# Performance work log

Hardware: AMD Instinct MI355X
Metric: run time of the kernel (lower is better)

## Reference

```python
import jax, jax.numpy as jnp
import numpy as np

B, L, E, H = 1, 2048, 512, 8
D = E // H


def setup_inputs() -> dict:
    key = jax.random.key(0)
    k0, k1, k2 = jax.random.split(key, 3)
    x = jax.random.normal(k0, (B, L, E), jnp.float32)
    W_qkv = jax.random.normal(k1, (E, 3 * E), jnp.float32) / np.sqrt(E).astype(np.float32)
    b_qkv = jnp.zeros((3 * E,), jnp.float32)
    W_out = jax.random.normal(k2, (E, E), jnp.float32) / np.sqrt(E).astype(np.float32)
    b_out = jnp.zeros((E,), jnp.float32)
    return {"x": x, "W_qkv": W_qkv, "b_qkv": b_qkv, "W_out": W_out, "b_out": b_out}


def reference(x, W_qkv, b_qkv, W_out, b_out):
    num_heads = H
    eps = 1e-6
    b, l, e = x.shape
    d = e // num_heads
    qkv = x @ W_qkv + b_qkv                      # [B, L, 3E]
    q, k, v = jnp.split(qkv, 3, axis=-1)
    q = q.reshape(b, l, num_heads, d).transpose(0, 2, 1, 3)  # [B,H,L,D]
    k = k.reshape(b, l, num_heads, d).transpose(0, 2, 1, 3)
    v = v.reshape(b, l, num_heads, d).transpose(0, 2, 1, 3)
    pos = jnp.arange(l, dtype=jnp.float32).reshape(1, 1, l, 1)
    cos_w = jnp.cos(jnp.pi / 2 * pos / l)
    sin_w = jnp.sin(jnp.pi / 2 * pos / l)
    q_prime = jax.nn.relu(q)
    k_prime = jax.nn.relu(k)

    def branch(w):
        qw = q_prime * w                          # [B,H,L,D]
        kw = k_prime * w
        kv = jnp.einsum('bhld,bhle->bhlde', kw, v)  # causal running KV state
        kv_cum = jnp.cumsum(kv, axis=2)
        ctx = jnp.einsum('bhld,bhlde->bhle', qw, kv_cum)
        nrm = jnp.einsum('bhld,bhld->bhl', qw, jnp.cumsum(kw, axis=2))
        return ctx, nrm

    ctx_cos, nrm_cos = branch(cos_w)
    ctx_sin, nrm_sin = branch(sin_w)
    out = (ctx_cos + ctx_sin) / ((nrm_cos + nrm_sin)[..., None] + eps)
    out = out.transpose(0, 2, 1, 3).reshape(b, l, e)
    return out @ W_out + b_out
```

## Files before the change

kernel.cpp:

```cpp
#include <hip/hip_runtime.h>

constexpr int L_SEQ = 2048;
constexpr int E_DIM = 512;
constexpr int H_NUM = 8;
constexpr int QKV_W = 3 * E_DIM;
constexpr int NC = 32;
constexpr float PI_HALF = 1.5707963267948966f;

typedef __attribute__((ext_vector_type(8))) short bf16x8;
typedef __attribute__((ext_vector_type(4))) float f32x4;
typedef __attribute__((ext_vector_type(4))) short short4v;

__device__ __forceinline__ short f2bf(float f) {
  union { float f; unsigned int u; } v; v.f = f;
  unsigned int r = v.u + 0x7fffu + ((v.u >> 16) & 1u);
  return (short)(r >> 16);
}
__device__ __forceinline__ float bf2f(short s) {
  union { unsigned int u; float f; } v;
  v.u = ((unsigned int)(unsigned short)s) << 16;
  return v.f;
}

__device__ __forceinline__ void glds16(const void* g, void* l) {
  __builtin_amdgcn_global_load_lds(
      (const __attribute__((address_space(1))) unsigned int*)g,
      (__attribute__((address_space(3))) unsigned int*)l, 16, 0, 0);
}

template <int WTM, int WTN, bool OB>
__global__ __launch_bounds__(256) void gemm_mfma_bf16(
    const short* __restrict__ A, const short* __restrict__ Bt,
    const float* __restrict__ bias, void* __restrict__ Cout,
    int M, int N, int K) {
  constexpr int BM = WTM * 32;
  constexpr int BN = WTN * 32;
  __shared__ short As[BM * 32];
  __shared__ short Bs[BN * 32];

  const int t = threadIdx.x;
  const int wave = t >> 6;
  const int lane = t & 63;
  const int quad = lane >> 4;
  const int lr = lane & 15;

  const int row0 = blockIdx.y * BM;
  const int col0 = blockIdx.x * BN;
  const int wrow = (wave >> 1) * (BM / 2);
  const int wcol = (wave & 1) * (BN / 2);

  f32x4 acc[WTM][WTN];
#pragma unroll
  for (int m = 0; m < WTM; ++m)
#pragma unroll
    for (int n = 0; n < WTN; ++n) acc[m][n] = (f32x4){0.f, 0.f, 0.f, 0.f};

  for (int k0 = 0; k0 < K; k0 += 32) {
#pragma unroll
    for (int p = wave; p < BM / 16; p += 4) {
      const int idx = p * 64 + lane;
      glds16(A + (size_t)(row0 + (idx >> 2)) * K + k0 + (idx & 3) * 8, As + p * 512);
    }
#pragma unroll
    for (int p = wave; p < BN / 16; p += 4) {
      const int idx = p * 64 + lane;
      glds16(Bt + (size_t)(col0 + (idx >> 2)) * K + k0 + (idx & 3) * 8, Bs + p * 512);
    }
    __syncthreads();

    bf16x8 af[WTM], bf_[WTN];
#pragma unroll
    for (int m = 0; m < WTM; ++m)
      af[m] = *(const bf16x8*)(As + (wrow + m * 16 + lr) * 32 + quad * 8);
#pragma unroll
    for (int n = 0; n < WTN; ++n)
      bf_[n] = *(const bf16x8*)(Bs + (wcol + n * 16 + lr) * 32 + quad * 8);
#pragma unroll
    for (int m = 0; m < WTM; ++m)
#pragma unroll
      for (int n = 0; n < WTN; ++n)
        acc[m][n] = __builtin_amdgcn_mfma_f32_16x16x32_bf16(af[m], bf_[n], acc[m][n], 0, 0, 0);
    __syncthreads();
  }

#pragma unroll
  for (int m = 0; m < WTM; ++m) {
#pragma unroll
    for (int n = 0; n < WTN; ++n) {
      const int col = col0 + wcol + n * 16 + lr;
      const int rowb = row0 + wrow + m * 16 + quad * 4;
      const float bb = bias[col];
#pragma unroll
      for (int r = 0; r < 4; ++r) {
        const float val = acc[m][n][r] + bb;
        if (OB)
          ((short*)Cout)[(size_t)(rowb + r) * N + col] = f2bf(val);
        else
          ((float*)Cout)[(size_t)(rowb + r) * N + col] = val;
      }
    }
  }
}

__global__ __launch_bounds__(256) void prep_kernel(
    const float* __restrict__ x, const float* __restrict__ W_qkv,
    const float* __restrict__ W_out, short* __restrict__ xb,
    short* __restrict__ Wqkv_t, short* __restrict__ Wout_t) {
  const int b = blockIdx.x;
  if (b < 1024) {
    const int i = b * 256 + threadIdx.x;
    const float4 v = ((const float4*)x)[i];
    short4v o;
    o.x = f2bf(v.x); o.y = f2bf(v.y); o.z = f2bf(v.z); o.w = f2bf(v.w);
    ((short4v*)xb)[i] = o;
    return;
  }
  __shared__ float tile[32][33];
  const float* W; short* Wt; int R, Cc, c0, r0;
  if (b < 1792) {
    const int bb = b - 1024;
    W = W_qkv; Wt = Wqkv_t; R = E_DIM; Cc = QKV_W;
    c0 = (bb % 48) * 32; r0 = (bb / 48) * 32;
  } else {
    const int bb = b - 1792;
    W = W_out; Wt = Wout_t; R = E_DIM; Cc = E_DIM;
    c0 = (bb % 16) * 32; r0 = (bb / 16) * 32;
  }
  const int tx = threadIdx.x & 31, ty = threadIdx.x >> 5;
  for (int i = ty; i < 32; i += 8) tile[i][tx] = W[(size_t)(r0 + i) * Cc + c0 + tx];
  __syncthreads();
  for (int i = ty; i < 32; i += 8)
    Wt[(size_t)(c0 + i) * R + r0 + tx] = f2bf(tile[tx][i]);
}

__global__ __launch_bounds__(256) void chunk_kv_mfma(
    const short* __restrict__ qkvb, short* __restrict__ Sb, float* __restrict__ ksum) {
  const int c = blockIdx.x, h = blockIdx.y;
  __shared__ short kT[128][72];
  __shared__ short vT[64][72];
  const int t = threadIdx.x;
  const int w = t >> 6, lane = t & 63, lr = lane & 15, quad = lane >> 4;

#pragma unroll
  for (int r = 0; r < 16; ++r) {
    const int i = w + 4 * r, d = lane;
    const short* row = qkvb + (size_t)(c * 64 + i) * QKV_W;
    const float kv_ = fmaxf(bf2f(row[E_DIM + h * 64 + d]), 0.f);
    const float v_ = bf2f(row[2 * E_DIM + h * 64 + d]);
    const float th = PI_HALF * (float)(c * 64 + i) / (float)L_SEQ;
    kT[d][i] = f2bf(kv_ * __cosf(th));
    kT[64 + d][i] = f2bf(kv_ * __sinf(th));
    vT[d][i] = f2bf(v_);
  }
  __syncthreads();

  f32x4 acc[8];
#pragma unroll
  for (int n = 0; n < 8; ++n) acc[n] = (f32x4){0.f, 0.f, 0.f, 0.f};
#pragma unroll
  for (int kk = 0; kk < 2; ++kk) {
    const bf16x8 av = *(const bf16x8*)&vT[16 * w + lr][kk * 32 + quad * 8];
#pragma unroll
    for (int n = 0; n < 8; ++n) {
      const bf16x8 bv = *(const bf16x8*)&kT[16 * n + lr][kk * 32 + quad * 8];
      acc[n] = __builtin_amdgcn_mfma_f32_16x16x32_bf16(av, bv, acc[n], 0, 0, 0);
    }
  }

  short* Sc = Sb + ((size_t)(h * NC + c)) * 8192;
#pragma unroll
  for (int n = 0; n < 8; ++n) {
    const int dd = 16 * n + lr;
#pragma unroll
    for (int r = 0; r < 4; ++r) {
      const int e = 16 * w + quad * 4 + r;
      Sc[(size_t)e * 128 + dd] = f2bf(acc[n][r]);
    }
  }

  if (t < 128) {
    float s = 0.f;
#pragma unroll
    for (int j = 0; j < 8; ++j) {
      const bf16x8 kv8 = *(const bf16x8*)&kT[t][j * 8];
#pragma unroll
      for (int q = 0; q < 8; ++q) s += bf2f(kv8[q]);
    }
    ksum[(size_t)(h * NC + c) * 128 + t] = s;
  }
}

__global__ __launch_bounds__(256) void scan_kernel(
    const short* __restrict__ Sb, short* __restrict__ Spb,
    const float* __restrict__ ksum, float* __restrict__ ksumP) {
  const int h = blockIdx.y;
  const int g = (blockIdx.x * 256 + threadIdx.x) * 8;
  float run[8];
#pragma unroll
  for (int q = 0; q < 8; ++q) run[q] = 0.f;
#pragma unroll
  for (int c = 0; c < NC; ++c) {
    const size_t off = ((size_t)(h * NC + c)) * 8192 + g;
    const bf16x8 v8 = *(const bf16x8*)(Sb + off);
    bf16x8 o;
#pragma unroll
    for (int q = 0; q < 8; ++q) o[q] = f2bf(run[q]);
    *(bf16x8*)(Spb + off) = o;
#pragma unroll
    for (int q = 0; q < 8; ++q) run[q] += bf2f(v8[q]);
  }
  if (blockIdx.x == 0 && threadIdx.x < 128) {
    const int d = threadIdx.x;
    float r2 = 0.f;
#pragma unroll
    for (int c = 0; c < NC; ++c) {
      const size_t off = (size_t)(h * NC + c) * 128 + d;
      ksumP[off] = r2;
      r2 += ksum[off];
    }
  }
}

__global__ __launch_bounds__(256) void chunk_out_mfma(
    const short* __restrict__ qkvb, const short* __restrict__ Spb,
    const float* __restrict__ ksumP, short* __restrict__ attn) {
  const int c = blockIdx.x, h = blockIdx.y;
  __shared__ short Qc[64][136];
  __shared__ short Kc[64][136];
  __shared__ short Am[64][72];
  __shared__ short vT[64][72];
  __shared__ float nrmP[64][4];
  __shared__ float nrmA[64];
  const int t = threadIdx.x;
  const int w = t >> 6, lane = t & 63, lr = lane & 15, quad = lane >> 4;

#pragma unroll
  for (int r = 0; r < 16; ++r) {
    const int i = w + 4 * r, d = lane;
    const short* row = qkvb + (size_t)(c * 64 + i) * QKV_W;
    const float q_ = fmaxf(bf2f(row[h * 64 + d]), 0.f);
    const float k_ = fmaxf(bf2f(row[E_DIM + h * 64 + d]), 0.f);
    const float v_ = bf2f(row[2 * E_DIM + h * 64 + d]);
    const float th = PI_HALF * (float)(c * 64 + i) / (float)L_SEQ;
    const float cw = __cosf(th), sw = __sinf(th);
    Qc[i][d] = f2bf(q_ * cw);
    Qc[i][64 + d] = f2bf(q_ * sw);
    Kc[i][d] = f2bf(k_ * cw);
    Kc[i][64 + d] = f2bf(k_ * sw);
    vT[d][i] = f2bf(v_);
  }
  __syncthreads();

  bf16x8 av[4];
#pragma unroll
  for (int kk = 0; kk < 4; ++kk)
    av[kk] = *(const bf16x8*)&Qc[16 * w + lr][kk * 32 + quad * 8];

  const short* Spc = Spb + ((size_t)(h * NC + c)) * 8192;
  f32x4 acc_c[4];
#pragma unroll
  for (int n = 0; n < 4; ++n) acc_c[n] = (f32x4){0.f, 0.f, 0.f, 0.f};
#pragma unroll
  for (int kk = 0; kk < 4; ++kk) {
#pragma unroll
    for (int n = 0; n < 4; ++n) {
      const bf16x8 bv = *(const bf16x8*)(Spc + (size_t)(16 * n + lr) * 128 + kk * 32 + quad * 8);
      acc_c[n] = __builtin_amdgcn_mfma_f32_16x16x32_bf16(av[kk], bv, acc_c[n], 0, 0, 0);
    }
  }

  f32x4 acc_a[4];
#pragma unroll
  for (int n = 0; n < 4; ++n) acc_a[n] = (f32x4){0.f, 0.f, 0.f, 0.f};
#pragma unroll
  for (int kk = 0; kk < 4; ++kk) {
#pragma unroll
    for (int n = 0; n < 4; ++n) {
      const bf16x8 bv = *(const bf16x8*)&Kc[16 * n + lr][kk * 32 + quad * 8];
      acc_a[n] = __builtin_amdgcn_mfma_f32_16x16x32_bf16(av[kk], bv, acc_a[n], 0, 0, 0);
    }
  }
#pragma unroll
  for (int n = 0; n < 4; ++n) {
#pragma unroll
    for (int r = 0; r < 4; ++r) {
      const int gi = 16 * w + quad * 4 + r;
      const int gj = 16 * n + lr;
      float val = (gj <= gi) ? acc_a[n][r] : 0.f;
      Am[gi][gj] = f2bf(val);
      float s = val;
      s += __shfl_xor(s, 1, 64);
      s += __shfl_xor(s, 2, 64);
      s += __shfl_xor(s, 4, 64);
      s += __shfl_xor(s, 8, 64);
      if (lr == 0) nrmP[gi][n] = s;
    }
  }
  __syncthreads();

#pragma unroll
  for (int kk = 0; kk < 2; ++kk) {
    const bf16x8 am = *(const bf16x8*)&Am[16 * w + lr][kk * 32 + quad * 8];
#pragma unroll
    for (int n = 0; n < 4; ++n) {
      const bf16x8 bv = *(const bf16x8*)&vT[16 * n + lr][kk * 32 + quad * 8];
      acc_c[n] = __builtin_amdgcn_mfma_f32_16x16x32_bf16(am, bv, acc_c[n], 0, 0, 0);
    }
  }

  {
    const int i = t >> 2, p = t & 3;
    const float* Kp = ksumP + (size_t)(h * NC + c) * 128;
    float dot = 0.f;
#pragma unroll
    for (int jj = 0; jj < 32; ++jj) {
      const int dd = p * 32 + jj;
      dot += bf2f(Qc[i][dd]) * Kp[dd];
    }
    nrmP[i][p] += dot;
  }
  __syncthreads();
  if (t < 64) nrmA[t] = nrmP[t][0] + nrmP[t][1] + nrmP[t][2] + nrmP[t][3];
  __syncthreads();

#pragma unroll
  for (int n = 0; n < 4; ++n) {
#pragma unroll
    for (int r = 0; r < 4; ++r) {
      const int gi = 16 * w + quad * 4 + r;
      const int e = 16 * n + lr;
      const float val = acc_c[n][r] / (nrmA[gi] + 1e-6f);
      attn[(size_t)(c * 64 + gi) * E_DIM + h * 64 + e] = f2bf(val);
    }
  }
}

extern "C" void kernel_launch(void* const* d_in, const int* in_sizes, int n_in,
                              void* d_out, int out_size, void* d_ws, size_t ws_size,
                              hipStream_t stream) {
  (void)in_sizes; (void)n_in; (void)out_size; (void)ws_size;
  const float* x     = (const float*)d_in[0];
  const float* W_qkv = (const float*)d_in[1];
  const float* b_qkv = (const float*)d_in[2];
  const float* W_out = (const float*)d_in[3];
  const float* b_out = (const float*)d_in[4];
  float* out = (float*)d_out;

  short* sws = (short*)d_ws;
  short* qkvb   = sws;
  short* Sb     = qkvb + 3145728;
  short* Spb    = Sb + 2097152;
  short* attn_b = Spb + 2097152;
  short* xb     = attn_b + 1048576;
  short* Wqkv_t = xb + 1048576;
  short* Wout_t = Wqkv_t + 786432;
  float* ksum   = (float*)(Wout_t + 262144);
  float* ksumP  = ksum + 32768;

  prep_kernel<<<2048, 256, 0, stream>>>(x, W_qkv, W_out, xb, Wqkv_t, Wout_t);

  gemm_mfma_bf16<2, 2, true><<<dim3(QKV_W / 64, L_SEQ / 64), 256, 0, stream>>>(
      xb, Wqkv_t, b_qkv, qkvb, L_SEQ, QKV_W, E_DIM);

  chunk_kv_mfma<<<dim3(NC, H_NUM), 256, 0, stream>>>(qkvb, Sb, ksum);

  scan_kernel<<<dim3(4, H_NUM), 256, 0, stream>>>(Sb, Spb, ksum, ksumP);

  chunk_out_mfma<<<dim3(NC, H_NUM), 256, 0, stream>>>(qkvb, Spb, ksumP, attn_b);

  gemm_mfma_bf16<1, 2, false><<<dim3(E_DIM / 64, L_SEQ / 32), 256, 0, stream>>>(
      attn_b, Wout_t, b_out, out, L_SEQ, E_DIM, E_DIM);
}
```

Baseline: 109.7 us.

## Split chunk KV and output kernels across a half dimension with vectorized loads

The chunk KV-state kernel and the chunk output kernel now launch twice as many blocks. The KV kernel splits the cos and sin halves across blocks, and the output kernel splits the value columns. Staging loads now use 8-wide bf16 vector reads with a single sincos call instead of scalar per-element loads. The aim is better occupancy of the many CUs on a small 256-block grid and cheaper global loads, at the cost of the output kernel recomputing the Q·K intra-chunk matrix and normalizer in both halves.

```diff
diff --git a/kernel.cpp b/kernel.cpp
--- a/kernel.cpp
+++ b/kernel.cpp
@@ -39,11 +39,7 @@
   __shared__ short Bs[BN * 32];
 
   const int t = threadIdx.x;
-  const int wave = t >> 6;
-  const int lane = t & 63;
-  const int quad = lane >> 4;
-  const int lr = lane & 15;
-
+  const int wave = t >> 6, lane = t & 63, quad = lane >> 4, lr = lane & 15;
   const int row0 = blockIdx.y * BM;
   const int col0 = blockIdx.x * BN;
   const int wrow = (wave >> 1) * (BM / 2);
@@ -116,69 +112,72 @@
     return;
   }
   __shared__ float tile[32][33];
-  const float* W; short* Wt; int R, Cc, c0, r0;
+  const float* W; short* Wt; int Cc, c0, r0;
   if (b < 1792) {
     const int bb = b - 1024;
-    W = W_qkv; Wt = Wqkv_t; R = E_DIM; Cc = QKV_W;
+    W = W_qkv; Wt = Wqkv_t; Cc = QKV_W;
     c0 = (bb % 48) * 32; r0 = (bb / 48) * 32;
   } else {
     const int bb = b - 1792;
-    W = W_out; Wt = Wout_t; R = E_DIM; Cc = E_DIM;
+    W = W_out; Wt = Wout_t; Cc = E_DIM;
     c0 = (bb % 16) * 32; r0 = (bb / 16) * 32;
   }
   const int tx = threadIdx.x & 31, ty = threadIdx.x >> 5;
   for (int i = ty; i < 32; i += 8) tile[i][tx] = W[(size_t)(r0 + i) * Cc + c0 + tx];
   __syncthreads();
   for (int i = ty; i < 32; i += 8)
-    Wt[(size_t)(c0 + i) * R + r0 + tx] = f2bf(tile[tx][i]);
-}
-
-__global__ __launch_bounds__(256) void chunk_kv_mfma(
+    Wt[(size_t)(c0 + i) * E_DIM + r0 + tx] = f2bf(tile[tx][i]);
+}
+
+__global__ __launch_bounds__(256) void chunk_kv_half(
     const short* __restrict__ qkvb, short* __restrict__ Sb, float* __restrict__ ksum) {
-  const int c = blockIdx.x, h = blockIdx.y;
-  __shared__ short kT[128][72];
+  const int c = blockIdx.x, h = blockIdx.y, half = blockIdx.z;
+  __shared__ short kT[64][72];
   __shared__ short vT[64][72];
   const int t = threadIdx.x;
-  const int w = t >> 6, lane = t & 63, lr = lane & 15, quad = lane >> 4;
-
-#pragma unroll
-  for (int r = 0; r < 16; ++r) {
-    const int i = w + 4 * r, d = lane;
-    const short* row = qkvb + (size_t)(c * 64 + i) * QKV_W;
-    const float kv_ = fmaxf(bf2f(row[E_DIM + h * 64 + d]), 0.f);
-    const float v_ = bf2f(row[2 * E_DIM + h * 64 + d]);
-    const float th = PI_HALF * (float)(c * 64 + i) / (float)L_SEQ;
-    kT[d][i] = f2bf(kv_ * __cosf(th));
-    kT[64 + d][i] = f2bf(kv_ * __sinf(th));
-    vT[d][i] = f2bf(v_);
-  }
-  __syncthreads();
-
-  f32x4 acc[8];
-#pragma unroll
-  for (int n = 0; n < 8; ++n) acc[n] = (f32x4){0.f, 0.f, 0.f, 0.f};
+  const int wave = t >> 6, lane = t & 63, quad = lane >> 4, lr = lane & 15;
+
+#pragma unroll
+  for (int r = 0; r < 2; ++r) {
+    const int idx = r * 256 + t;
+    const int i = idx >> 3, dg = idx & 7;
+    const short* row = qkvb + (size_t)(c * 64 + i) * QKV_W + h * 64 + dg * 8;
+    const bf16x8 kb = *(const bf16x8*)(row + E_DIM);
+    const bf16x8 vb = *(const bf16x8*)(row + 2 * E_DIM);
+    float sw, cw;
+    __sincosf(PI_HALF * (float)(c * 64 + i) / (float)L_SEQ, &sw, &cw);
+    const float wgt = half ? sw : cw;
+#pragma unroll
+    for (int q = 0; q < 8; ++q) {
+      kT[dg * 8 + q][i] = f2bf(fmaxf(bf2f(kb[q]), 0.f) * wgt);
+      vT[dg * 8 + q][i] = vb[q];
+    }
+  }
+  __syncthreads();
+
+  f32x4 sacc[4];
+#pragma unroll
+  for (int n = 0; n < 4; ++n) sacc[n] = (f32x4){0.f, 0.f, 0.f, 0.f};
 #pragma unroll
   for (int kk = 0; kk < 2; ++kk) {
-    const bf16x8 av = *(const bf16x8*)&vT[16 * w + lr][kk * 32 + quad * 8];
-#pragma unroll
-    for (int n = 0; n < 8; ++n) {
+    const bf16x8 av = *(const bf16x8*)&vT[16 * wave + lr][kk * 32 + quad * 8];
+#pragma unroll
+    for (int n = 0; n < 4; ++n) {
       const bf16x8 bv = *(const bf16x8*)&kT[16 * n + lr][kk * 32 + quad * 8];
-      acc[n] = __builtin_amdgcn_mfma_f32_16x16x32_bf16(av, bv, acc[n], 0, 0, 0);
-    }
-  }
-
+      sacc[n] = __builtin_amdgcn_mfma_f32_16x16x32_bf16(av, bv, sacc[n], 0, 0, 0);
+    }
+  }
   short* Sc = Sb + ((size_t)(h * NC + c)) * 8192;
 #pragma unroll
-  for (int n = 0; n < 8; ++n) {
-    const int dd = 16 * n + lr;
+  for (int n = 0; n < 4; ++n) {
+    const int dd = 64 * half + 16 * n + lr;
 #pragma unroll
     for (int r = 0; r < 4; ++r) {
-      const int e = 16 * w + quad * 4 + r;
-      Sc[(size_t)e * 128 + dd] = f2bf(acc[n][r]);
-    }
-  }
-
-  if (t < 128) {
+      const int e = 16 * wave + quad * 4 + r;
+      Sc[(size_t)e * 128 + dd] = f2bf(sacc[n][r]);
+    }
+  }
+  if (t < 64) {
     float s = 0.f;
 #pragma unroll
     for (int j = 0; j < 8; ++j) {
@@ -186,7 +185,7 @@
 #pragma unroll
       for (int q = 0; q < 8; ++q) s += bf2f(kv8[q]);
     }
-    ksum[(size_t)(h * NC + c) * 128 + t] = s;
+    ksum[(size_t)(h * NC + c) * 128 + 64 * half + t] = s;
   }
 }
 
@@ -221,53 +220,55 @@
   }
 }
 
-__global__ __launch_bounds__(256) void chunk_out_mfma(
+__global__ __launch_bounds__(256) void chunk_out_half(
     const short* __restrict__ qkvb, const short* __restrict__ Spb,
     const float* __restrict__ ksumP, short* __restrict__ attn) {
-  const int c = blockIdx.x, h = blockIdx.y;
+  const int c = blockIdx.x, h = blockIdx.y, eh = blockIdx.z;
   __shared__ short Qc[64][136];
   __shared__ short Kc[64][136];
   __shared__ short Am[64][72];
-  __shared__ short vT[64][72];
+  __shared__ short vT[32][72];
   __shared__ float nrmP[64][4];
   __shared__ float nrmA[64];
   const int t = threadIdx.x;
-  const int w = t >> 6, lane = t & 63, lr = lane & 15, quad = lane >> 4;
-
-#pragma unroll
-  for (int r = 0; r < 16; ++r) {
-    const int i = w + 4 * r, d = lane;
-    const short* row = qkvb + (size_t)(c * 64 + i) * QKV_W;
-    const float q_ = fmaxf(bf2f(row[h * 64 + d]), 0.f);
-    const float k_ = fmaxf(bf2f(row[E_DIM + h * 64 + d]), 0.f);
-    const float v_ = bf2f(row[2 * E_DIM + h * 64 + d]);
-    const float th = PI_HALF * (float)(c * 64 + i) / (float)L_SEQ;
-    const float cw = __cosf(th), sw = __sinf(th);
-    Qc[i][d] = f2bf(q_ * cw);
-    Qc[i][64 + d] = f2bf(q_ * sw);
-    Kc[i][d] = f2bf(k_ * cw);
-    Kc[i][64 + d] = f2bf(k_ * sw);
-    vT[d][i] = f2bf(v_);
+  const int wave = t >> 6, lane = t & 63, quad = lane >> 4, lr = lane & 15;
+
+#pragma unroll
+  for (int r = 0; r < 2; ++r) {
+    const int idx = r * 256 + t;
+    const int i = idx >> 3, dg = idx & 7;
+    const short* row = qkvb + (size_t)(c * 64 + i) * QKV_W + h * 64 + dg * 8;
+    const bf16x8 qb = *(const bf16x8*)row;
+    const bf16x8 kb = *(const bf16x8*)(row + E_DIM);
+    float sw, cw;
+    __sincosf(PI_HALF * (float)(c * 64 + i) / (float)L_SEQ, &sw, &cw);
+    bf16x8 qc, qs, kc, ks;
+#pragma unroll
+    for (int q = 0; q < 8; ++q) {
+      const float qv = fmaxf(bf2f(qb[q]), 0.f);
+      const float kv = fmaxf(bf2f(kb[q]), 0.f);
+      qc[q] = f2bf(qv * cw); qs[q] = f2bf(qv * sw);
+      kc[q] = f2bf(kv * cw); ks[q] = f2bf(kv * sw);
+    }
+    *(bf16x8*)&Qc[i][dg * 8] = qc;
+    *(bf16x8*)&Qc[i][64 + dg * 8] = qs;
+    *(bf16x8*)&Kc[i][dg * 8] = kc;
+    *(bf16x8*)&Kc[i][64 + dg * 8] = ks;
+  }
+  {
+    const int i = t >> 2, dg = (t & 3) + 4 * eh;
+    const bf16x8 vb = *(const bf16x8*)(qkvb + (size_t)(c * 64 + i) * QKV_W +
+                                       2 * E_DIM + h * 64 + dg * 8);
+    const int el0 = (dg - 4 * eh) * 8;
+#pragma unroll
+    for (int q = 0; q < 8; ++q) vT[el0 + q][i] = vb[q];
   }
   __syncthreads();
 
   bf16x8 av[4];
 #pragma unroll
   for (int kk = 0; kk < 4; ++kk)
-    av[kk] = *(const bf16x8*)&Qc[16 * w + lr][kk * 32 + quad * 8];
-
-  const short* Spc = Spb + ((size_t)(h * NC + c)) * 8192;
-  f32x4 acc_c[4];
-#pragma unroll
-  for (int n = 0; n < 4; ++n) acc_c[n] = (f32x4){0.f, 0.f, 0.f, 0.f};
-#pragma unroll
-  for (int kk = 0; kk < 4; ++kk) {
-#pragma unroll
-    for (int n = 0; n < 4; ++n) {
-      const bf16x8 bv = *(const bf16x8*)(Spc + (size_t)(16 * n + lr) * 128 + kk * 32 + quad * 8);
-      acc_c[n] = __builtin_amdgcn_mfma_f32_16x16x32_bf16(av[kk], bv, acc_c[n], 0, 0, 0);
-    }
-  }
+    av[kk] = *(const bf16x8*)&Qc[16 * wave + lr][kk * 32 + quad * 8];
 
   f32x4 acc_a[4];
 #pragma unroll
@@ -284,7 +285,7 @@
   for (int n = 0; n < 4; ++n) {
 #pragma unroll
     for (int r = 0; r < 4; ++r) {
-      const int gi = 16 * w + quad * 4 + r;
+      const int gi = 16 * wave + quad * 4 + r;
       const int gj = 16 * n + lr;
       float val = (gj <= gi) ? acc_a[n][r] : 0.f;
       Am[gi][gj] = f2bf(val);
@@ -296,15 +297,29 @@
       if (lr == 0) nrmP[gi][n] = s;
     }
   }
+
+  const short* Spc = Spb + ((size_t)(h * NC + c)) * 8192;
+  f32x4 acc_c[2];
+#pragma unroll
+  for (int n = 0; n < 2; ++n) acc_c[n] = (f32x4){0.f, 0.f, 0.f, 0.f};
+#pragma unroll
+  for (int kk = 0; kk < 4; ++kk) {
+#pragma unroll
+    for (int n2 = 0; n2 < 2; ++n2) {
+      const int e = 32 * eh + 16 * n2 + lr;
+      const bf16x8 bv = *(const bf16x8*)(Spc + (size_t)e * 128 + kk * 32 + quad * 8);
+      acc_c[n2] = __builtin_amdgcn_mfma_f32_16x16x32_bf16(av[kk], bv, acc_c[n2], 0, 0, 0);
+    }
+  }
   __syncthreads();
 
 #pragma unroll
   for (int kk = 0; kk < 2; ++kk) {
-    const bf16x8 am = *(const bf16x8*)&Am[16 * w + lr][kk * 32 + quad * 8];
-#pragma unroll
-    for (int n = 0; n < 4; ++n) {
-      const bf16x8 bv = *(const bf16x8*)&vT[16 * n + lr][kk * 32 + quad * 8];
-      acc_c[n] = __builtin_amdgcn_mfma_f32_16x16x32_bf16(am, bv, acc_c[n], 0, 0, 0);
+    const bf16x8 am = *(const bf16x8*)&Am[16 * wave + lr][kk * 32 + quad * 8];
+#pragma unroll
+    for (int n2 = 0; n2 < 2; ++n2) {
+      const bf16x8 bv = *(const bf16x8*)&vT[16 * n2 + lr][kk * 32 + quad * 8];
+      acc_c[n2] = __builtin_amdgcn_mfma_f32_16x16x32_bf16(am, bv, acc_c[n2], 0, 0, 0);
     }
   }
 
@@ -324,12 +339,12 @@
   __syncthreads();
 
 #pragma unroll
-  for (int n = 0; n < 4; ++n) {
+  for (int n2 = 0; n2 < 2; ++n2) {
 #pragma unroll
     for (int r = 0; r < 4; ++r) {
-      const int gi = 16 * w + quad * 4 + r;
-      const int e = 16 * n + lr;
-      const float val = acc_c[n][r] / (nrmA[gi] + 1e-6f);
+      const int gi = 16 * wave + quad * 4 + r;
+      const int e = 32 * eh + 16 * n2 + lr;
+      const float val = acc_c[n2][r] / (nrmA[gi] + 1e-6f);
       attn[(size_t)(c * 64 + gi) * E_DIM + h * 64 + e] = f2bf(val);
     }
   }
@@ -362,11 +377,11 @@
   gemm_mfma_bf16<2, 2, true><<<dim3(QKV_W / 64, L_SEQ / 64), 256, 0, stream>>>(
       xb, Wqkv_t, b_qkv, qkvb, L_SEQ, QKV_W, E_DIM);
 
-  chunk_kv_mfma<<<dim3(NC, H_NUM), 256, 0, stream>>>(qkvb, Sb, ksum);
+  chunk_kv_half<<<dim3(NC, H_NUM, 2), 256, 0, stream>>>(qkvb, Sb, ksum);
 
   scan_kernel<<<dim3(4, H_NUM), 256, 0, stream>>>(Sb, Spb, ksum, ksumP);
 
-  chunk_out_mfma<<<dim3(NC, H_NUM), 256, 0, stream>>>(qkvb, Spb, ksumP, attn_b);
+  chunk_out_half<<<dim3(NC, H_NUM, 2), 256, 0, stream>>>(qkvb, Spb, ksumP, attn_b);
 
   gemm_mfma_bf16<1, 2, false><<<dim3(E_DIM / 64, L_SEQ / 32), 256, 0, stream>>>(
       attn_b, Wout_t, b_out, out, L_SEQ, E_DIM, E_DIM);
```

Measured after the change: 110.0 us. No clear change (+0.2%).
